# Kernel optimization log

Hardware: AMD Instinct MI355X
Metric: run time of the kernel (lower is better)

## Reference

```python
import jax, jax.numpy as jnp
import numpy as np

N_NODES = 100000
N_EDGES = 1600000
IN_DIM, HID_DIM, OUT_DIM = 256, 64, 64
EPS = 1e-12  # F.normalize eps


def _gcn_conv(x, src, dst, norm, W, b, num_nodes):
    # PyG-style GCNConv: transform, then symmetric-normalized aggregation.
    h = x @ W                                   # [N, d_out]
    msg = norm[:, None] * h[src]                # [E+N, d_out] gathered messages
    out = jax.ops.segment_sum(msg, dst, num_segments=num_nodes)
    return out + b


def _l2_normalize(h):
    # F.normalize(h, p=2, dim=1)
    n = jnp.sqrt(jnp.sum(h * h, axis=-1, keepdims=True))
    return h / jnp.maximum(n, EPS)


def setup_inputs() -> dict:
    key = jax.random.key(0)
    ks = jax.random.split(key, 8)
    x = jax.random.normal(ks[0], (N_NODES, IN_DIM), dtype=jnp.float32)
    edge_index = jax.random.randint(ks[1], (2, N_EDGES), 0, N_NODES, dtype=jnp.int64)
    def glorot(k, fan_in, fan_out):
        s = np.sqrt(6.0 / (fan_in + fan_out)).astype(np.float32)
        return jax.random.uniform(k, (fan_in, fan_out), jnp.float32, -s, s)
    W1 = glorot(ks[2], IN_DIM, HID_DIM)
    W2 = glorot(ks[3], HID_DIM, HID_DIM)
    W3 = glorot(ks[4], HID_DIM, OUT_DIM)
    b1 = jnp.zeros((HID_DIM,), jnp.float32)
    b2 = jnp.zeros((HID_DIM,), jnp.float32)
    b3 = jnp.zeros((OUT_DIM,), jnp.float32)
    return {"x": x, "edge_index": edge_index,
            "W1": W1, "b1": b1, "W2": W2, "b2": b2, "W3": W3, "b3": b3}


def reference(x, edge_index, W1, b1, W2, b2, W3, b3):
    N = x.shape[0]
    # add self-loops and compute symmetric norm D^-1/2 A_hat D^-1/2
    loop = jnp.arange(N, dtype=edge_index.dtype)
    src = jnp.concatenate([edge_index[0], loop])
    dst = jnp.concatenate([edge_index[1], loop])
    deg = jax.ops.segment_sum(jnp.ones_like(src, dtype=x.dtype), dst, num_segments=N)
    dinv = jnp.where(deg > 0, jax.lax.rsqrt(jnp.maximum(deg, 1.0)), 0.0)
    norm = dinv[src] * dinv[dst]                # [E+N]

    # layer 1: conv -> relu -> (dropout p=0 = identity) -> L2-normalize
    h = jax.nn.relu(_gcn_conv(x, src, dst, norm, W1, b1, N))
    h = _l2_normalize(h)
    # layer 2
    h = jax.nn.relu(_gcn_conv(h, src, dst, norm, W2, b2, N))
    h = _l2_normalize(h)
    # final layer: plain conv (cast to float32, already float32)
    out = _gcn_conv(h, src, dst, norm, W3, b3, N)
    return out
```

## Files before the change

kernel.cpp:

```cpp
#include <hip/hip_runtime.h>
#include <hip/hip_bf16.h>
#include <math.h>

#define HID 64
#define KT 64

#define NBBITS 10
#define NBSZ 1024
#define P1_BMAX 128
#define P1_CH 4096
#define P1_CAP 96

typedef __attribute__((ext_vector_type(8))) short s16x8;
typedef __attribute__((ext_vector_type(4))) float f32x4;

static inline size_t align256(size_t x) { return (x + 255) & ~(size_t)255; }

__device__ inline void gld_lds16(const float* g, float* lds) {
  __builtin_amdgcn_global_load_lds((const __attribute__((address_space(1))) void*)g,
                                   (__attribute__((address_space(3))) void*)lds, 16, 0, 0);
}

__device__ inline unsigned short f2bf(float f) {
  unsigned u = __float_as_uint(f);
  return (unsigned short)((u + 0x7FFFu + ((u >> 16) & 1u)) >> 16);
}
__device__ inline float bf2f(unsigned short h) { return __uint_as_float(((unsigned)h) << 16); }
__device__ inline float bf_lo(unsigned int u) { return __uint_as_float(u << 16); }
__device__ inline float bf_hi(unsigned int u) { return __uint_as_float(u & 0xffff0000u); }


__global__ void count_dst_kernel(const int* __restrict__ dst, int* __restrict__ cnt, int E) {
  int e = blockIdx.x * blockDim.x + threadIdx.x;
  if (e < E) atomicAdd(&cnt[dst[e]], 1);
}

__global__ void dinv_kernel(const int* __restrict__ cnt, float* __restrict__ dinv, int N) {
  int i = blockIdx.x * blockDim.x + threadIdx.x;
  if (i < N) dinv[i] = rsqrtf((float)(cnt[i] + 1));
}


__global__ void bucket_count_kernel(const int* __restrict__ dst, int* __restrict__ bcnt,
                                    int E, int B) {
  __shared__ int sh[1024];
  for (int i = threadIdx.x; i < B; i += blockDim.x) sh[i] = 0;
  __syncthreads();
  for (int e = blockIdx.x * blockDim.x + threadIdx.x; e < E; e += gridDim.x * blockDim.x)
    atomicAdd(&sh[dst[e] >> NBBITS], 1);
  __syncthreads();
  for (int i = threadIdx.x; i < B; i += blockDim.x) {
    int v = sh[i];
    if (v) atomicAdd(&bcnt[i], v);
  }
}

__global__ __launch_bounds__(1024) void bucket_scan_kernel(const int* __restrict__ bcnt,
                                                           int* __restrict__ bbase,
                                                           int* __restrict__ gcur, int B) {
  __shared__ int sh[1024];
  int t = threadIdx.x;
  int v = (t < B) ? bcnt[t] : 0;
  sh[t] = v;
  __syncthreads();
  for (int off = 1; off < 1024; off <<= 1) {
    int u = (t >= off) ? sh[t - off] : 0;
    __syncthreads();
    sh[t] += u;
    __syncthreads();
  }
  if (t < B) {
    int ex = sh[t] - v;
    bbase[t] = ex;
    gcur[t] = ex;
  }
  if (t == 1023) bbase[B] = sh[1023];
}

__global__ __launch_bounds__(256) void bucketize_kernel(const int* __restrict__ src,
                                                        const int* __restrict__ dst,
                                                        int* __restrict__ gcur,
                                                        int* __restrict__ ebuck, int E) {
  __shared__ int cnt[P1_BMAX];
  __shared__ int lists[P1_BMAX * P1_CAP];
  int t = threadIdx.x;
  for (int i = t; i < P1_BMAX; i += 256) cnt[i] = 0;
  __syncthreads();
  int base_e = blockIdx.x * P1_CH;
#pragma unroll
  for (int u = 0; u < P1_CH / 256; ++u) {
    int e = base_e + u * 256 + t;
    if (e < E) {
      int s = src[e], d = dst[e];
      int bk = d >> NBBITS;
      int packed = (s << NBBITS) | (d & (NBSZ - 1));
      int p = atomicAdd(&cnt[bk], 1);
      if (p < P1_CAP) {
        lists[bk * P1_CAP + p] = packed;
      } else {
        int gp = atomicAdd(&gcur[bk], 1);
        ebuck[gp] = packed;
      }
    }
  }
  __syncthreads();
  int w = t >> 6, lane = t & 63;
  int bk = w * 32 + (lane & 31);
  int c = min(cnt[bk], P1_CAP);
  int mybase = 0;
  if (lane < 32 && c > 0) mybase = atomicAdd(&gcur[bk], c);
#pragma unroll 1
  for (int i = 0; i < 32; ++i) {
    int cb = __shfl(c, i);
    if (cb == 0) continue;
    int gb = __shfl(mybase, i);
    int bb = w * 32 + i;
    if (lane < cb) ebuck[gb + lane] = lists[bb * P1_CAP + lane];
    if (cb > 64 && lane < cb - 64) ebuck[gb + 64 + lane] = lists[bb * P1_CAP + 64 + lane];
  }
}

__global__ __launch_bounds__(1024) void bucket_sort_kernel(const int* __restrict__ ebuck,
                                                           const int* __restrict__ bbase,
                                                           int* __restrict__ rowptr,
                                                           int* __restrict__ epack,
                                                           float* __restrict__ dinv,
                                                           int N, int B, int E) {
  __shared__ int lcnt[NBSZ];
  __shared__ int lcur[NBSZ];
  int b = blockIdx.x;
  int t = threadIdx.x;
  int n0 = b << NBBITS;
  lcnt[t] = 0;
  __syncthreads();
  int e0 = bbase[b], e1 = bbase[b + 1];
  for (int i = e0 + t; i < e1; i += 1024) atomicAdd(&lcnt[ebuck[i] & (NBSZ - 1)], 1);
  __syncthreads();
  int v = lcnt[t];
  for (int off = 1; off < 1024; off <<= 1) {
    int u = (t >= off) ? lcnt[t - off] : 0;
    __syncthreads();
    lcnt[t] += u;
    __syncthreads();
  }
  int ex = lcnt[t] - v;
  int node = n0 + t;
  if (node < N) {
    rowptr[node] = e0 + ex;
    dinv[node] = rsqrtf((float)(v + 1));
  }
  if (b == B - 1 && t == 0) rowptr[N] = E;
  lcur[t] = e0 + ex;
  __syncthreads();
  for (int i = e0 + t; i < e1; i += 1024) {
    int pv = ebuck[i];
    int pos = atomicAdd(&lcur[pv & (NBSZ - 1)], 1);
    epack[pos] = ((unsigned)pv) >> NBBITS;
  }
}


__global__ void wprep_kernel(const float* __restrict__ W1, const float* __restrict__ W2,
                             const float* __restrict__ W3, unsigned short* __restrict__ W1h,
                             unsigned short* __restrict__ W1l, unsigned short* __restrict__ W2h,
                             unsigned short* __restrict__ W2l, unsigned short* __restrict__ W3h,
                             unsigned short* __restrict__ W3l) {
  int b = blockIdx.x, t = threadIdx.x;
  const float* W;
  unsigned short *Dh, *Dl;
  int idx;
  if (b < 64)      { W = W1; Dh = W1h; Dl = W1l; idx = b * 256 + t; }
  else if (b < 80) { W = W2; Dh = W2h; Dl = W2l; idx = (b - 64) * 256 + t; }
  else             { W = W3; Dh = W3h; Dl = W3l; idx = (b - 80) * 256 + t; }
  int j = idx & 7, lane = (idx >> 3) & 63, ct = (idx >> 9) & 3, s = idx >> 11;
  int k = s * 32 + ((lane >> 4) << 3) + j;
  int col = ct * 16 + (lane & 15);
  float f = W[k * HID + col];
  unsigned short h = f2bf(f);
  Dh[idx] = h;
  Dl[idx] = f2bf(f - bf2f(h));
}


template <int K>
__global__ __launch_bounds__(256, 4) void gemm_mfma_kernel(
    const float* __restrict__ x, const unsigned short* __restrict__ Wh,
    const unsigned short* __restrict__ Wl, const float* __restrict__ dinv,
    unsigned short* __restrict__ out, int N) {
  constexpr int NS = K / 32;
  __shared__ float xs[2][64 * 32];
  const int t = threadIdx.x, lane = t & 63, w = t >> 6;
  const int g = lane >> 4, r15 = lane & 15;
  const int row0 = blockIdx.x * 64;
  const int arow = w * 16 + r15;
  f32x4 acc[4];
#pragma unroll
  for (int ct = 0; ct < 4; ++ct) acc[ct] = (f32x4){0.f, 0.f, 0.f, 0.f};

  auto stage = [&](int buf, int s) {
#pragma unroll
    for (int c = 0; c < 2; ++c) {
      int idx = c * 256 + t;
      int row = idx >> 3, gp = idx & 7;
      int gs = gp ^ (row & 7);
      int grow = min(row0 + row, N - 1);
      gld_lds16(x + (size_t)grow * K + s * 32 + gs * 4, &xs[buf][idx * 4]);
    }
  };
  stage(0, 0);
  for (int s = 0; s < NS; ++s) {
    __syncthreads();
    if (s + 1 < NS) stage((s + 1) & 1, s + 1);
    const float* xb = &xs[s & 1][arow * 32];
    float4 xv0 = *(const float4*)&xb[((2 * g) ^ (arow & 7)) * 4];
    float4 xv1 = *(const float4*)&xb[((2 * g + 1) ^ (arow & 7)) * 4];
    float xf[8] = {xv0.x, xv0.y, xv0.z, xv0.w, xv1.x, xv1.y, xv1.z, xv1.w};
    s16x8 xh, xl;
#pragma unroll
    for (int j = 0; j < 8; ++j) {
      unsigned short hb = f2bf(xf[j]);
      xh[j] = (short)hb;
      xl[j] = (short)f2bf(xf[j] - bf2f(hb));
    }
#pragma unroll
    for (int ct = 0; ct < 4; ++ct) {
      size_t o = (((size_t)(s * 4 + ct)) * 64 + lane) * 8;
      s16x8 wh = *(const s16x8*)&Wh[o];
      s16x8 wl = *(const s16x8*)&Wl[o];
      acc[ct] = __builtin_amdgcn_mfma_f32_16x16x32_bf16(wh, xh, acc[ct], 0, 0, 0);
      acc[ct] = __builtin_amdgcn_mfma_f32_16x16x32_bf16(wl, xh, acc[ct], 0, 0, 0);
      acc[ct] = __builtin_amdgcn_mfma_f32_16x16x32_bf16(wh, xl, acc[ct], 0, 0, 0);
    }
  }
  int row = row0 + arow;
  if (row < N) {
    float di = dinv[row];
    unsigned short* orow = out + (size_t)row * HID;
#pragma unroll
    for (int ct = 0; ct < 4; ++ct) {
      unsigned p0 = (unsigned)f2bf(di * acc[ct][0]) | ((unsigned)f2bf(di * acc[ct][1]) << 16);
      unsigned p1 = (unsigned)f2bf(di * acc[ct][2]) | ((unsigned)f2bf(di * acc[ct][3]) << 16);
      *(uint2*)&orow[ct * 16 + g * 4] = make_uint2(p0, p1);
    }
  }
}


template <bool RELU_NORM>
__global__ void agg_kernel(const int* __restrict__ rowptr, const int* __restrict__ ep,
                           const float* __restrict__ dinv, const uint2* __restrict__ h64,
                           const float* __restrict__ bias, float* __restrict__ out, int N) {
  int grp = (blockIdx.x * blockDim.x + threadIdx.x) >> 6;
  int lane = threadIdx.x & 63;
  int q = lane >> 4;
  int sub = lane & 15;
  int node = grp * 4 + q;
  if (node >= N) return;
  int beg = rowptr[node];
  int end = rowptr[node + 1];
  uint2 su = h64[(size_t)node * 16 + sub];
  float a0 = bf_lo(su.x), a1 = bf_hi(su.x), a2 = bf_lo(su.y), a3 = bf_hi(su.y);
  int j = beg;
  for (; j + 8 <= end; j += 8) {
    int e[8];
    uint2 hv[8];
#pragma unroll
    for (int u = 0; u < 8; ++u) e[u] = ep[j + u];
#pragma unroll
    for (int u = 0; u < 8; ++u) hv[u] = h64[(size_t)e[u] * 16 + sub];
#pragma unroll
    for (int u = 0; u < 8; ++u) {
      a0 += bf_lo(hv[u].x); a1 += bf_hi(hv[u].x);
      a2 += bf_lo(hv[u].y); a3 += bf_hi(hv[u].y);
    }
  }
  for (; j < end; ++j) {
    uint2 hu = h64[(size_t)ep[j] * 16 + sub];
    a0 += bf_lo(hu.x); a1 += bf_hi(hu.x); a2 += bf_lo(hu.y); a3 += bf_hi(hu.y);
  }
  float di = dinv[node];
  float4 b4 = *(const float4*)&bias[sub * 4];
  float4 v;
  v.x = fmaf(di, a0, b4.x); v.y = fmaf(di, a1, b4.y);
  v.z = fmaf(di, a2, b4.z); v.w = fmaf(di, a3, b4.w);
  if (RELU_NORM) {
    v.x = fmaxf(v.x, 0.f); v.y = fmaxf(v.y, 0.f);
    v.z = fmaxf(v.z, 0.f); v.w = fmaxf(v.w, 0.f);
    float ss = v.x * v.x + v.y * v.y + v.z * v.z + v.w * v.w;
#pragma unroll
    for (int off = 8; off; off >>= 1) ss += __shfl_xor(ss, off, 64);
    float inv = 1.f / fmaxf(sqrtf(ss), 1e-12f);
    v.x *= inv; v.y *= inv; v.z *= inv; v.w *= inv;
  }
  *(float4*)&out[(size_t)node * HID + sub * 4] = v;
}


template <int K, typename OT>
__global__ __launch_bounds__(256, 4) void gemm_kernel(const float* __restrict__ x,
                                                      const float* __restrict__ W,
                                                      OT* __restrict__ out, int N) {
  __shared__ float Xs[64 * KT];
  __shared__ float Ws[KT * 64];
  const int t = threadIdx.x;
  const int lane = t & 63;
  const int w = t >> 6;
  const int rg = lane >> 4;
  const int cg = lane & 15;
  const int row0 = blockIdx.x * 64;
  float4 acc[4];
#pragma unroll
  for (int r = 0; r < 4; ++r) acc[r] = make_float4(0.f, 0.f, 0.f, 0.f);

  for (int k0 = 0; k0 < K; k0 += KT) {
    if (k0) __syncthreads();
    const float* Wg = W + (size_t)k0 * HID;
#pragma unroll
    for (int c = 0; c < 4; ++c) {
      int idx = c * 256 + t;
      gld_lds16(Wg + idx * 4, &Ws[idx * 4]);
      int srow = idx >> 4;
      int sg = (idx & 15) ^ ((srow >> 2) & 3);
      int grow = min(row0 + srow, N - 1);
      gld_lds16(x + (size_t)grow * K + k0 + (sg << 2), &Xs[idx * 4]);
    }
    __syncthreads();
    const int rbase = w * 16 + rg * 4;
#pragma unroll 4
    for (int kb = 0; kb < KT / 4; ++kb) {
      float4 wq0 = *(const float4*)&Ws[(4 * kb + 0) * HID + cg * 4];
      float4 wq1 = *(const float4*)&Ws[(4 * kb + 1) * HID + cg * 4];
      float4 wq2 = *(const float4*)&Ws[(4 * kb + 2) * HID + cg * 4];
      float4 wq3 = *(const float4*)&Ws[(4 * kb + 3) * HID + cg * 4];
      const int sg = (kb ^ rg) << 2;
#pragma unroll
      for (int r = 0; r < 4; ++r) {
        float4 xv = *(const float4*)&Xs[(rbase + r) * KT + sg];
        acc[r].x = fmaf(xv.w, wq3.x, fmaf(xv.z, wq2.x, fmaf(xv.y, wq1.x, fmaf(xv.x, wq0.x, acc[r].x))));
        acc[r].y = fmaf(xv.w, wq3.y, fmaf(xv.z, wq2.y, fmaf(xv.y, wq1.y, fmaf(xv.x, wq0.y, acc[r].y))));
        acc[r].z = fmaf(xv.w, wq3.z, fmaf(xv.z, wq2.z, fmaf(xv.y, wq1.z, fmaf(xv.x, wq0.z, acc[r].z))));
        acc[r].w = fmaf(xv.w, wq3.w, fmaf(xv.z, wq2.w, fmaf(xv.y, wq1.w, fmaf(xv.x, wq0.w, acc[r].w))));
      }
    }
  }
#pragma unroll
  for (int r = 0; r < 4; ++r) {
    int row = row0 + w * 16 + rg * 4 + r;
    if (row < N) {
      OT* o = out + (size_t)row * HID + cg * 4;
      o[0] = (OT)acc[r].x; o[1] = (OT)acc[r].y; o[2] = (OT)acc[r].z; o[3] = (OT)acc[r].w;
    }
  }
}


__global__ void init_agg_kernel(const float* __restrict__ dinv, const float* __restrict__ h,
                                const float* __restrict__ bias, float* __restrict__ out, int N) {
  int t = blockIdx.x * blockDim.x + threadIdx.x;
  int i = t >> 6, f = t & 63;
  if (i >= N) return;
  float di = dinv[i];
  out[t] = di * di * h[t] + bias[f];
}

__global__ void edge_atomic_kernel(const int* __restrict__ src, const int* __restrict__ dst,
                                   const float* __restrict__ dinv, const float* __restrict__ h,
                                   float* __restrict__ out, int E) {
  int t = blockIdx.x * blockDim.x + threadIdx.x;
  int e = t >> 6;
  if (e >= E) return;
  int f = t & 63;
  int s = src[e], d = dst[e];
  atomicAdd(&out[(size_t)d * HID + f], dinv[s] * dinv[d] * h[(size_t)s * HID + f]);
}

__global__ void relu_norm_kernel(float* __restrict__ hbuf, int N) {
  int t = blockIdx.x * blockDim.x + threadIdx.x;
  int i = t >> 6;
  if (i >= N) return;
  float v = fmaxf(hbuf[t], 0.f);
  float ss = v * v;
#pragma unroll
  for (int off = 32; off; off >>= 1) ss += __shfl_xor(ss, off, 64);
  hbuf[t] = v / fmaxf(sqrtf(ss), 1e-12f);
}


extern "C" void kernel_launch(void* const* d_in, const int* in_sizes, int n_in,
                              void* d_out, int out_size, void* d_ws, size_t ws_size,
                              hipStream_t stream) {
  const float* x  = (const float*)d_in[0];
  const int*   ei = (const int*)d_in[1];
  const float* W1 = (const float*)d_in[2];
  const float* b1 = (const float*)d_in[3];
  const float* W2 = (const float*)d_in[4];
  const float* b2 = (const float*)d_in[5];
  const float* W3 = (const float*)d_in[6];
  const float* b3 = (const float*)d_in[7];
  float* out = (float*)d_out;

  const int IN = in_sizes[2] / HID;
  const int N  = in_sizes[0] / IN;
  const int E  = in_sizes[1] / 2;
  const int* srcI = ei;
  const int* dstI = ei + E;
  const int B = (N + NBSZ - 1) >> NBBITS;

  char* w = (char*)d_ws;
  size_t off = 0;
  auto alloc = [&](size_t bytes) { void* p = w + off; off = align256(off + bytes); return p; };
  float* A      = (float*)alloc((size_t)N * HID * 4);
  float* dinv   = (float*)alloc((size_t)N * 4);
  int*   cnt    = (int*)alloc((size_t)N * 4);
  size_t base_need = off;
  int*   rowptr = (int*)alloc((size_t)(N + 1) * 4);
  int*   epack  = (int*)alloc((size_t)E * 4);
  int*   bbase  = (int*)alloc(1032 * 4);
  int*   gcur   = (int*)alloc(1024 * 4);
  int*   bcnt   = (int*)alloc(1024 * 4);
  unsigned short* W1h = (unsigned short*)alloc(16384 * 2);
  unsigned short* W1l = (unsigned short*)alloc(16384 * 2);
  unsigned short* W2h = (unsigned short*)alloc(4096 * 2);
  unsigned short* W2l = (unsigned short*)alloc(4096 * 2);
  unsigned short* W3h = (unsigned short*)alloc(4096 * 2);
  unsigned short* W3l = (unsigned short*)alloc(4096 * 2);
  size_t csr_need = off;

  if (base_need > ws_size) return;
  const bool use_csr = (csr_need <= ws_size) && (B <= P1_BMAX) &&
                       ((size_t)E <= (size_t)N * HID) && (N <= (1 << 20));
  uint2* Ab64 = (uint2*)A;
  unsigned short* Abs = (unsigned short*)A;
  int* ebuck = (int*)A;

  const int blkE    = (E + 255) / 256;
  const int blkN    = (N + 255) / 256;
  const int blkRow  = (N + 63) / 64;
  const int blkWave = (N * 64 + 255) / 256;
  const int blkAgg  = ((size_t)((N + 3) / 4) * 64 + 255) / 256;
  const int blkEF   = ((size_t)E * 64 + 255) / 256;
  const int blkBkt  = (E + P1_CH - 1) / P1_CH;

  if (use_csr) {
    hipMemsetAsync(bcnt, 0, 1024 * 4, stream);
    wprep_kernel<<<96, 256, 0, stream>>>(W1, W2, W3, W1h, W1l, W2h, W2l, W3h, W3l);
    bucket_count_kernel<<<256, 256, 0, stream>>>(dstI, bcnt, E, B);
    bucket_scan_kernel<<<1, 1024, 0, stream>>>(bcnt, bbase, gcur, B);
    bucketize_kernel<<<blkBkt, 256, 0, stream>>>(srcI, dstI, gcur, ebuck, E);
    bucket_sort_kernel<<<B, 1024, 0, stream>>>(ebuck, bbase, rowptr, epack, dinv, N, B, E);

    gemm_mfma_kernel<256><<<blkRow, 256, 0, stream>>>(x, W1h, W1l, dinv, Abs, N);
    agg_kernel<true><<<blkAgg, 256, 0, stream>>>(rowptr, epack, dinv, Ab64, b1, out, N);
    gemm_mfma_kernel<64><<<blkRow, 256, 0, stream>>>(out, W2h, W2l, dinv, Abs, N);
    agg_kernel<true><<<blkAgg, 256, 0, stream>>>(rowptr, epack, dinv, Ab64, b2, out, N);
    gemm_mfma_kernel<64><<<blkRow, 256, 0, stream>>>(out, W3h, W3l, dinv, Abs, N);
    agg_kernel<false><<<blkAgg, 256, 0, stream>>>(rowptr, epack, dinv, Ab64, b3, out, N);
  } else {
    hipMemsetAsync(cnt, 0, (size_t)N * 4, stream);
    count_dst_kernel<<<blkE, 256, 0, stream>>>(dstI, cnt, E);
    dinv_kernel<<<blkN, 256, 0, stream>>>(cnt, dinv, N);

    gemm_kernel<256><<<blkRow, 256, 0, stream>>>(x, W1, A, N);
    init_agg_kernel<<<blkWave, 256, 0, stream>>>(dinv, A, b1, out, N);
    edge_atomic_kernel<<<blkEF, 256, 0, stream>>>(srcI, dstI, dinv, A, out, E);
    relu_norm_kernel<<<blkWave, 256, 0, stream>>>(out, N);

    gemm_kernel<64><<<blkRow, 256, 0, stream>>>(out, W2, A, N);
    init_agg_kernel<<<blkWave, 256, 0, stream>>>(dinv, A, b2, out, N);
    edge_atomic_kernel<<<blkEF, 256, 0, stream>>>(srcI, dstI, dinv, A, out, E);
    relu_norm_kernel<<<blkWave, 256, 0, stream>>>(out, N);

    gemm_kernel<64><<<blkRow, 256, 0, stream>>>(out, W3, A, N);
    init_agg_kernel<<<blkWave, 256, 0, stream>>>(dinv, A, b3, out, N);
    edge_atomic_kernel<<<blkEF, 256, 0, stream>>>(srcI, dstI, dinv, A, out, E);
  }
}
```

Measured before the change: 387.2 us.

## Fuse aggregation with next layer's 64x64 transform in one kernel

Adds a kernel that gathers neighbour features in CSR order, then applies bias, ReLU and L2 normalisation, and multiplies the normalised row by the next layer's weight matrix. The weight matrix is held in fp32 in LDS and the product is scaled by dinv and stored as bf16. This replaces the separate MFMA GEMM launches for layers 2 and 3 and the fp32 intermediate round-trip through global memory, using ping-pong bf16 buffers. The cost is about 20 KB of LDS per 16-node block, which may limit occupancy, and the small GEMM now runs as scalar FMAs instead of split-bf16 MFMA.

```diff
diff --git a/kernel.cpp b/kernel.cpp
--- a/kernel.cpp
+++ b/kernel.cpp
@@ -160,18 +160,9 @@
 }
 
 
-__global__ void wprep_kernel(const float* __restrict__ W1, const float* __restrict__ W2,
-                             const float* __restrict__ W3, unsigned short* __restrict__ W1h,
-                             unsigned short* __restrict__ W1l, unsigned short* __restrict__ W2h,
-                             unsigned short* __restrict__ W2l, unsigned short* __restrict__ W3h,
-                             unsigned short* __restrict__ W3l) {
-  int b = blockIdx.x, t = threadIdx.x;
-  const float* W;
-  unsigned short *Dh, *Dl;
-  int idx;
-  if (b < 64)      { W = W1; Dh = W1h; Dl = W1l; idx = b * 256 + t; }
-  else if (b < 80) { W = W2; Dh = W2h; Dl = W2l; idx = (b - 64) * 256 + t; }
-  else             { W = W3; Dh = W3h; Dl = W3l; idx = (b - 80) * 256 + t; }
+__global__ void wprep_kernel(const float* __restrict__ W, unsigned short* __restrict__ Dh,
+                             unsigned short* __restrict__ Dl) {
+  int idx = blockIdx.x * 256 + threadIdx.x;
   int j = idx & 7, lane = (idx >> 3) & 63, ct = (idx >> 9) & 3, s = idx >> 11;
   int k = s * 32 + ((lane >> 4) << 3) + j;
   int col = ct * 16 + (lane & 15);
@@ -242,6 +233,81 @@
       unsigned p1 = (unsigned)f2bf(di * acc[ct][2]) | ((unsigned)f2bf(di * acc[ct][3]) << 16);
       *(uint2*)&orow[ct * 16 + g * 4] = make_uint2(p0, p1);
     }
+  }
+}
+
+
+__global__ __launch_bounds__(256) void agg_gemm_kernel(
+    const int* __restrict__ rowptr, const int* __restrict__ ep,
+    const float* __restrict__ dinv, const uint2* __restrict__ hin,
+    const float* __restrict__ bias, const float* __restrict__ Wn,
+    unsigned short* __restrict__ hout, int N) {
+  __shared__ float Ws[64 * 64];
+  __shared__ float vrow[16 * 65];
+  const int t = threadIdx.x;
+#pragma unroll
+  for (int c = 0; c < 4; ++c) {
+    int idx = c * 256 + t;
+    gld_lds16(Wn + idx * 4, &Ws[idx * 4]);
+  }
+  const int w = t >> 6, lane = t & 63;
+  const int q = lane >> 4, sub = lane & 15;
+  const int lr = w * 4 + q;
+  const int node = blockIdx.x * 16 + lr;
+  const bool act = node < N;
+  float di = 0.f;
+  if (act) {
+    int beg = rowptr[node];
+    int end = rowptr[node + 1];
+    uint2 su = hin[(size_t)node * 16 + sub];
+    float a0 = bf_lo(su.x), a1 = bf_hi(su.x), a2 = bf_lo(su.y), a3 = bf_hi(su.y);
+    int j = beg;
+    for (; j + 8 <= end; j += 8) {
+      int e[8];
+      uint2 hv[8];
+#pragma unroll
+      for (int u = 0; u < 8; ++u) e[u] = ep[j + u];
+#pragma unroll
+      for (int u = 0; u < 8; ++u) hv[u] = hin[(size_t)e[u] * 16 + sub];
+#pragma unroll
+      for (int u = 0; u < 8; ++u) {
+        a0 += bf_lo(hv[u].x); a1 += bf_hi(hv[u].x);
+        a2 += bf_lo(hv[u].y); a3 += bf_hi(hv[u].y);
+      }
+    }
+    for (; j < end; ++j) {
+      uint2 hu = hin[(size_t)ep[j] * 16 + sub];
+      a0 += bf_lo(hu.x); a1 += bf_hi(hu.x); a2 += bf_lo(hu.y); a3 += bf_hi(hu.y);
+    }
+    di = dinv[node];
+    float4 b4 = *(const float4*)&bias[sub * 4];
+    float4 v;
+    v.x = fmaxf(fmaf(di, a0, b4.x), 0.f);
+    v.y = fmaxf(fmaf(di, a1, b4.y), 0.f);
+    v.z = fmaxf(fmaf(di, a2, b4.z), 0.f);
+    v.w = fmaxf(fmaf(di, a3, b4.w), 0.f);
+    float ss = v.x * v.x + v.y * v.y + v.z * v.z + v.w * v.w;
+#pragma unroll
+    for (int off = 8; off; off >>= 1) ss += __shfl_xor(ss, off, 64);
+    float inv = 1.f / fmaxf(sqrtf(ss), 1e-12f);
+    v.x *= inv; v.y *= inv; v.z *= inv; v.w *= inv;
+    *(float4*)&vrow[lr * 65 + sub * 4] = v;
+  }
+  __syncthreads();
+  if (act) {
+    float4 o = make_float4(0.f, 0.f, 0.f, 0.f);
+#pragma unroll 8
+    for (int f = 0; f < 64; ++f) {
+      float vf = vrow[lr * 65 + f];
+      float4 wf = *(const float4*)&Ws[f * 64 + sub * 4];
+      o.x = fmaf(vf, wf.x, o.x);
+      o.y = fmaf(vf, wf.y, o.y);
+      o.z = fmaf(vf, wf.z, o.z);
+      o.w = fmaf(vf, wf.w, o.w);
+    }
+    unsigned p0 = (unsigned)f2bf(di * o.x) | ((unsigned)f2bf(di * o.y) << 16);
+    unsigned p1 = (unsigned)f2bf(di * o.z) | ((unsigned)f2bf(di * o.w) << 16);
+    *(uint2*)&hout[(size_t)node * HID + sub * 4] = make_uint2(p0, p1);
   }
 }
 
@@ -420,17 +486,13 @@
   int*   bcnt   = (int*)alloc(1024 * 4);
   unsigned short* W1h = (unsigned short*)alloc(16384 * 2);
   unsigned short* W1l = (unsigned short*)alloc(16384 * 2);
-  unsigned short* W2h = (unsigned short*)alloc(4096 * 2);
-  unsigned short* W2l = (unsigned short*)alloc(4096 * 2);
-  unsigned short* W3h = (unsigned short*)alloc(4096 * 2);
-  unsigned short* W3l = (unsigned short*)alloc(4096 * 2);
   size_t csr_need = off;
 
   if (base_need > ws_size) return;
   const bool use_csr = (csr_need <= ws_size) && (B <= P1_BMAX) &&
                        ((size_t)E <= (size_t)N * HID) && (N <= (1 << 20));
-  uint2* Ab64 = (uint2*)A;
-  unsigned short* Abs = (unsigned short*)A;
+  unsigned short* hsA = (unsigned short*)A;
+  unsigned short* hsB = hsA + (size_t)N * HID;
   int* ebuck = (int*)A;
 
   const int blkE    = (E + 255) / 256;
@@ -438,23 +500,25 @@
   const int blkRow  = (N + 63) / 64;
   const int blkWave = (N * 64 + 255) / 256;
   const int blkAgg  = ((size_t)((N + 3) / 4) * 64 + 255) / 256;
+  const int blkFuse = (N + 15) / 16;
   const int blkEF   = ((size_t)E * 64 + 255) / 256;
   const int blkBkt  = (E + P1_CH - 1) / P1_CH;
 
   if (use_csr) {
     hipMemsetAsync(bcnt, 0, 1024 * 4, stream);
-    wprep_kernel<<<96, 256, 0, stream>>>(W1, W2, W3, W1h, W1l, W2h, W2l, W3h, W3l);
+    wprep_kernel<<<64, 256, 0, stream>>>(W1, W1h, W1l);
     bucket_count_kernel<<<256, 256, 0, stream>>>(dstI, bcnt, E, B);
     bucket_scan_kernel<<<1, 1024, 0, stream>>>(bcnt, bbase, gcur, B);
     bucketize_kernel<<<blkBkt, 256, 0, stream>>>(srcI, dstI, gcur, ebuck, E);
     bucket_sort_kernel<<<B, 1024, 0, stream>>>(ebuck, bbase, rowptr, epack, dinv, N, B, E);
 
-    gemm_mfma_kernel<256><<<blkRow, 256, 0, stream>>>(x, W1h, W1l, dinv, Abs, N);
-    agg_kernel<true><<<blkAgg, 256, 0, stream>>>(rowptr, epack, dinv, Ab64, b1, out, N);
-    gemm_mfma_kernel<64><<<blkRow, 256, 0, stream>>>(out, W2h, W2l, dinv, Abs, N);
-    agg_kernel<true><<<blkAgg, 256, 0, stream>>>(rowptr, epack, dinv, Ab64, b2, out, N);
-    gemm_mfma_kernel<64><<<blkRow, 256, 0, stream>>>(out, W3h, W3l, dinv, Abs, N);
-    agg_kernel<false><<<blkAgg, 256, 0, stream>>>(rowptr, epack, dinv, Ab64, b3, out, N);
+    gemm_mfma_kernel<256><<<blkRow, 256, 0, stream>>>(x, W1h, W1l, dinv, hsA, N);
+    agg_gemm_kernel<<<blkFuse, 256, 0, stream>>>(rowptr, epack, dinv, (const uint2*)hsA,
+                                                 b1, W2, hsB, N);
+    agg_gemm_kernel<<<blkFuse, 256, 0, stream>>>(rowptr, epack, dinv, (const uint2*)hsB,
+                                                 b2, W3, hsA, N);
+    agg_kernel<false><<<blkAgg, 256, 0, stream>>>(rowptr, epack, dinv, (const uint2*)hsA,
+                                                  b3, out, N);
   } else {
     hipMemsetAsync(cnt, 0, (size_t)N * 4, stream);
     count_dst_kernel<<<blkE, 256, 0, stream>>>(dstI, cnt, E);
```

Result: no change. 381.6 us (-1.5%).
